# Kernel optimization log

Hardware: AMD Instinct MI355X
Metric: run time of the kernel (lower is better)

The kernel has to match this reference:

```python
import jax, jax.numpy as jnp
import numpy as np

NJ = 24
COL = 14
TMP = 3  # gaussian half-window (tmp_size)


def _forward(o, h, o3D, h3D, t, t3D, v):
    B = h.shape[0]
    f32 = jnp.float32
    scale = 1.0 / COL
    cc = COL * COL

    # ---- 2D heatmap argmax decode: x[i,j] = offset at argmax + coord*scale ----
    am = jnp.argmax(h.reshape(B, NJ, cc), axis=-1)            # (B, Nj)
    y2 = am // COL
    x2 = am % COL
    of = o.reshape(B, 2 * NJ, cc)
    gx = jnp.take_along_axis(of[:, :NJ], am[..., None], axis=-1)[..., 0]
    gy = jnp.take_along_axis(of[:, NJ:], am[..., None], axis=-1)[..., 0]
    x2d = jnp.stack([gx + x2.astype(f32) * scale,
                     gy + y2.astype(f32) * scale], axis=-1)   # (B, Nj, 2)

    # ---- 3D heatmap argmax decode ----
    h3r = h3D.reshape(B, NJ, COL, COL, COL)                   # (B, Nj, z, y, x)
    am3 = jnp.argmax(h3r.reshape(B, NJ, COL ** 3), axis=-1)
    z3 = am3 // cc
    r3 = am3 % cc
    y3 = r3 // COL
    x3 = r3 % COL
    o3r = o3D.reshape(B, 3, NJ, COL ** 3)                     # 3 coord channels
    g0 = jnp.take_along_axis(o3r[:, 0], am3[..., None], axis=-1)[..., 0]
    g1 = jnp.take_along_axis(o3r[:, 1], am3[..., None], axis=-1)[..., 0]
    g2 = jnp.take_along_axis(o3r[:, 2], am3[..., None], axis=-1)[..., 0]
    x3d = jnp.stack([g0 + x3.astype(f32) * scale,
                     g1 + y3.astype(f32) * scale,
                     g2 + (z3 - 7).astype(f32) * scale], axis=-1)  # (B, Nj, 3)

    v0 = v[..., 0]
    vis = (v0 == 1)

    # ---- 2D gaussian target placement (torch int() == floor for t >= 0) ----
    mu_x = jnp.floor(t[..., 0] * COL + 0.5).astype(jnp.int32)
    mu_y = jnp.floor(t[..., 1] * COL + 0.5).astype(jnp.int32)
    valid2d = ~((mu_x - TMP >= COL) | (mu_y - TMP >= COL) |
                (mu_x + TMP + 1 <= 0) | (mu_y + TMP + 1 <= 0))
    coords = jnp.arange(COL, dtype=jnp.int32)
    dx = coords[None, None, :] - mu_x[..., None]              # (B, Nj, COL)
    dy = coords[None, None, :] - mu_y[..., None]
    in2 = (jnp.abs(dx) <= TMP)[:, :, None, :] & (jnp.abs(dy) <= TMP)[:, :, :, None]
    sq2 = (dx.astype(f32) ** 2)[:, :, None, :] + (dy.astype(f32) ** 2)[:, :, :, None]
    gate2 = (vis & valid2d)[..., None, None]
    tt = jnp.where(in2 & gate2, jnp.exp(-0.5 * sq2), 0.0)     # (B, Nj, COL, COL)

    # ---- 3D gaussian target placement (only checked when still visible) ----
    m3x = jnp.floor(t3D[..., 0] * COL + 0.5).astype(jnp.int32)
    m3y = jnp.floor(t3D[..., 1] * COL + 0.5).astype(jnp.int32)
    m3z = jnp.floor(t3D[..., 2] * COL + 7 + 0.5).astype(jnp.int32)
    valid3d = ~((m3x - TMP >= COL) | (m3y - TMP >= COL) | (m3z - TMP >= COL) |
                (m3x + TMP + 1 < 0) | (m3y + TMP + 1 < 0) | (m3z + TMP + 1 < 0))
    dX = coords[None, None, :] - m3x[..., None]
    dY = coords[None, None, :] - m3y[..., None]
    dZ = coords[None, None, :] - m3z[..., None]
    in3 = ((jnp.abs(dX) <= TMP)[:, :, None, None, :] &
           (jnp.abs(dY) <= TMP)[:, :, None, :, None] &
           (jnp.abs(dZ) <= TMP)[:, :, :, None, None])
    sq3 = ((dX.astype(f32) ** 2)[:, :, None, None, :] +
           (dY.astype(f32) ** 2)[:, :, None, :, None] +
           (dZ.astype(f32) ** 2)[:, :, :, None, None])
    vf_bool = vis & valid2d & valid3d                          # final visibility
    tt3 = jnp.where(in3 & vf_bool[..., None, None, None], jnp.exp(-0.5 * sq3), 0.0)

    # ---- visibility mutation: v zeroed when a visible joint's target is OOB ----
    keep = jnp.where(vis, valid2d & valid3d, True)
    v_f = v * keep[..., None].astype(f32)                      # (B, Nj, 3)
    # x3D was skipped (left 0) when the 2D check invalidated a visible joint
    x3d = x3d * (~(vis & ~valid2d))[..., None].astype(f32)

    vf0 = v_f[..., 0]
    jmask = (vf0 != 0).astype(f32)                             # (B, Nj)
    cnt = jnp.sum(jmask)
    Nv = jnp.sum(v_f) / 3.0

    diff1 = (h - tt) * jmask[..., None, None]
    d1 = jnp.sqrt(jnp.sum(diff1 * diff1)) / cnt

    diff2 = (x2d - t) * v_f[..., :2]
    d2 = jnp.sqrt(jnp.sum(diff2 * diff2)) / Nv

    diff3 = (h3r - tt3) * jmask[..., None, None, None]
    d3 = jnp.sqrt(jnp.sum(diff3 * diff3)) / cnt

    diff4 = (x3d - t3D) * v_f
    d4 = jnp.sqrt(jnp.sum(diff4 * diff4)) / Nv

    return d1 + d2 + d3 + d4


def setup_inputs() -> dict:
    B = 256
    key = jax.random.key(0)
    ks = jax.random.split(key, 7)
    o = 0.1 * jax.random.normal(ks[0], (B, 2 * NJ, COL, COL), jnp.float32)
    h = jax.random.normal(ks[1], (B, NJ, COL, COL), jnp.float32)
    o3D = 0.1 * jax.random.normal(ks[2], (B, 3 * NJ * COL, COL, COL), jnp.float32)
    h3D = jax.random.normal(ks[3], (B, NJ * COL, COL, COL), jnp.float32)
    t = jax.random.uniform(ks[4], (B, NJ, 2), jnp.float32)
    t3D = jax.random.uniform(ks[5], (B, NJ, 3), jnp.float32)
    v0 = jax.random.bernoulli(ks[6], 0.8, (B, NJ)).astype(jnp.float32)
    v = jnp.repeat(v0[..., None], 3, axis=-1)
    return {"o": o, "h": h, "o3D": o3D, "h3D": h3D, "t": t, "t3D": t3D,
            "v": v, "d": 0, "path": 0}


def reference(o, h, o3D, h3D, t, t3D, v, d, path):
    # d > -990 selects the full d1+d2+d3+d4 loss (static Python branch)
    return _forward(o, h, o3D, h3D, t, t3D, v)
```

## Files before the change

### kernel.cpp

```cpp
#include <hip/hip_runtime.h>
#include <float.h>
#include <math.h>

#define NJ   24
#define COL  14
#define CC   196
#define CC3  2744
#define NV4_3D 686
#define NV4_2D 49
#define TMPW 3

__global__ __launch_bounds__(64)
void msed_pair_kernel(const float* __restrict__ o,
                      const float* __restrict__ h,
                      const float* __restrict__ o3D,
                      const float* __restrict__ h3D,
                      const float* __restrict__ t,
                      const float* __restrict__ t3D,
                      const float* __restrict__ v,
                      float* __restrict__ part)
{
    const int pair = blockIdx.x;
    const int lane = threadIdx.x;

    const float tx  = t[pair * 2 + 0];
    const float ty  = t[pair * 2 + 1];
    const float t3x = t3D[pair * 3 + 0];
    const float t3y = t3D[pair * 3 + 1];
    const float t3z = t3D[pair * 3 + 2];
    const float v0  = v[pair * 3 + 0];
    const float v1  = v[pair * 3 + 1];
    const float v2c = v[pair * 3 + 2];
    const bool vis = (v0 == 1.0f);

    const int mux = (int)floorf(tx * (float)COL + 0.5f);
    const int muy = (int)floorf(ty * (float)COL + 0.5f);
    const bool valid2d = !((mux - TMPW >= COL) || (muy - TMPW >= COL) ||
                           (mux + TMPW + 1 <= 0) || (muy + TMPW + 1 <= 0));

    const int m3x = (int)floorf(t3x * (float)COL + 0.5f);
    const int m3y = (int)floorf(t3y * (float)COL + 0.5f);
    const int m3z = (int)floorf(t3z * (float)COL + 7.0f + 0.5f);
    const bool valid3d = !((m3x - TMPW >= COL) || (m3y - TMPW >= COL) || (m3z - TMPW >= COL) ||
                           (m3x + TMPW + 1 < 0) || (m3y + TMPW + 1 < 0) || (m3z + TMPW + 1 < 0));

    const float keep = vis ? ((valid2d && valid3d) ? 1.0f : 0.0f) : 1.0f;
    const float vf0 = v0 * keep, vf1 = v1 * keep, vf2 = v2c * keep;
    const bool jm     = (vf0 != 0.0f);
    const bool active = jm || (vf1 != 0.0f) || (vf2 != 0.0f);
    const bool gate2  = vis && valid2d;
    const bool gate3  = vis && valid2d && valid3d;

    if (!active) {
        if (lane == 0) {
            float4 z4 = make_float4(0.f, 0.f, 0.f, 0.f);
            *(float4*)(part + (size_t)pair * 8)     = z4;
            *(float4*)(part + (size_t)pair * 8 + 4) = z4;
        }
        return;
    }

    const float4* hp3 = (const float4*)(h3D + (size_t)pair * CC3);
    float s3 = 0.0f;
    float bv3 = -FLT_MAX; int bi3 = 0x7FFFFFFF;
    #pragma unroll
    for (int u = 0; u < 11; ++u) {
        const int i = lane + (u << 6);
        const bool valid = (u < 10) || (lane < (NV4_3D - 640));
        const int ic = valid ? i : lane;
        float4 q = hp3[ic];
        float vals[4] = {q.x, q.y, q.z, q.w};
        const int e0 = ic * 4;
        #pragma unroll
        for (int c = 0; c < 4; ++c) {
            float hv = vals[c];
            if (valid) {
                s3 += hv * hv;
                if (hv > bv3) { bv3 = hv; bi3 = e0 + c; }
            }
        }
    }

    float s1 = 0.0f;
    float bv2 = -FLT_MAX; int bi2 = 0x7FFFFFFF;
    if (lane < NV4_2D) {
        const float4* hp2 = (const float4*)(h + (size_t)pair * CC);
        float4 q = hp2[lane];
        float vals[4] = {q.x, q.y, q.z, q.w};
        const int e0 = lane * 4;
        #pragma unroll
        for (int c = 0; c < 4; ++c) {
            float hv = vals[c];
            s1 += hv * hv;
            if (hv > bv2) { bv2 = hv; bi2 = e0 + c; }
        }
    }

    if (lane < 49) {
        const int dx = lane % 7 - TMPW;
        const int dy = lane / 7 - TMPW;
        const float gxy = __expf(-0.5f * (float)(dx * dx + dy * dy));

        if (gate2) {
            const int x = mux + dx, y = muy + dy;
            if ((unsigned)x < COL && (unsigned)y < COL) {
                const float wh = h[(size_t)pair * CC + y * COL + x];
                s1 += gxy * (gxy - 2.0f * wh);
            }
        }
        if (gate3) {
            const int x = m3x + dx, y = m3y + dy;
            if ((unsigned)x < COL && (unsigned)y < COL) {
                const float* base = h3D + (size_t)pair * CC3 + y * COL + x;
                #pragma unroll
                for (int dz = -TMPW; dz <= TMPW; ++dz) {
                    const int z = m3z + dz;
                    if ((unsigned)z < COL) {
                        const float g = gxy * __expf(-0.5f * (float)(dz * dz));
                        const float wh = base[z * CC];
                        s3 += g * (g - 2.0f * wh);
                    }
                }
            }
        }
    }

    #pragma unroll
    for (int off = 32; off > 0; off >>= 1) {
        s3 += __shfl_down(s3, off);
        s1 += __shfl_down(s1, off);
        float ov = __shfl_down(bv3, off); int oi = __shfl_down(bi3, off);
        if (ov > bv3 || (ov == bv3 && oi < bi3)) { bv3 = ov; bi3 = oi; }
        float ow = __shfl_down(bv2, off); int oj = __shfl_down(bi2, off);
        if (ow > bv2 || (ow == bv2 && oj < bi2)) { bv2 = ow; bi2 = oj; }
    }

    if (lane == 0) {
        const int b = pair / NJ;
        const int j = pair - b * NJ;
        const float scale = 1.0f / (float)COL;

        const int am = bi2;
        const int x2 = am % COL, y2 = am / COL;
        float gx = o[((size_t)b * (2 * NJ) + j) * CC + am];
        float gy = o[((size_t)b * (2 * NJ) + NJ + j) * CC + am];
        float x2dx = gx + (float)x2 * scale;
        float x2dy = gy + (float)y2 * scale;

        const int am3 = bi3;
        const int z3 = am3 / CC; const int r3 = am3 - z3 * CC;
        const int y3 = r3 / COL; const int x3 = r3 - y3 * COL;
        size_t base3 = (size_t)b * (3 * NJ * CC3) + (size_t)j * CC3 + am3;
        float g0 = o3D[base3];
        float g1 = o3D[base3 + (size_t)NJ * CC3];
        float g2 = o3D[base3 + (size_t)(2 * NJ) * CC3];
        float x3dx = g0 + (float)x3 * scale;
        float x3dy = g1 + (float)y3 * scale;
        float x3dz = g2 + (float)(z3 - 7) * scale;
        if (vis && !valid2d) { x3dx = 0.f; x3dy = 0.f; x3dz = 0.f; }

        float d2x = (x2dx - tx) * vf0;
        float d2y = (x2dy - ty) * vf1;
        float s2 = d2x * d2x + d2y * d2y;

        float d4x = (x3dx - t3x) * vf0;
        float d4y = (x3dy - t3y) * vf1;
        float d4z = (x3dz - t3z) * vf2;
        float s4 = d4x * d4x + d4y * d4y + d4z * d4z;

        float jmf = jm ? 1.0f : 0.0f;
        float4 p0 = make_float4(jm ? s1 : 0.f, s2, jm ? s3 : 0.f, s4);
        float4 p1 = make_float4(jmf, vf0 + vf1 + vf2, 0.f, 0.f);
        *(float4*)(part + (size_t)pair * 8)     = p0;
        *(float4*)(part + (size_t)pair * 8 + 4) = p1;
    }
}

__global__ __launch_bounds__(1024)
void msed_reduce_kernel(const float* __restrict__ part, int npairs,
                        float* __restrict__ out)
{
    const int tid = threadIdx.x;
    double a0 = 0, a1 = 0, a2 = 0, a3 = 0, a4 = 0, a5 = 0;
    for (int p = tid; p < npairs; p += 1024) {
        const float4 q0 = *(const float4*)(part + (size_t)p * 8);
        const float4 q1 = *(const float4*)(part + (size_t)p * 8 + 4);
        a0 += (double)q0.x; a1 += (double)q0.y; a2 += (double)q0.z; a3 += (double)q0.w;
        a4 += (double)q1.x; a5 += (double)q1.y;
    }

    #pragma unroll
    for (int off = 32; off > 0; off >>= 1) {
        a0 += __shfl_down(a0, off);
        a1 += __shfl_down(a1, off);
        a2 += __shfl_down(a2, off);
        a3 += __shfl_down(a3, off);
        a4 += __shfl_down(a4, off);
        a5 += __shfl_down(a5, off);
    }

    __shared__ double ws[16][6];
    const int wave = tid >> 6;
    if ((tid & 63) == 0) {
        ws[wave][0] = a0; ws[wave][1] = a1; ws[wave][2] = a2;
        ws[wave][3] = a3; ws[wave][4] = a4; ws[wave][5] = a5;
    }
    __syncthreads();

    if (tid == 0) {
        #pragma unroll
        for (int w = 1; w < 16; ++w) {
            a0 += ws[w][0]; a1 += ws[w][1]; a2 += ws[w][2];
            a3 += ws[w][3]; a4 += ws[w][4]; a5 += ws[w][5];
        }
        double cnt = a4;
        double Nv  = a5 / 3.0;
        float d1 = (float)(sqrt(a0) / cnt);
        float d2 = (float)(sqrt(a1) / Nv);
        float d3 = (float)(sqrt(a2) / cnt);
        float d4 = (float)(sqrt(a3) / Nv);
        out[0] = d1 + d2 + d3 + d4;
    }
}

extern "C" void kernel_launch(void* const* d_in, const int* in_sizes, int n_in,
                              void* d_out, int out_size, void* d_ws, size_t ws_size,
                              hipStream_t stream)
{
    const float* o   = (const float*)d_in[0];
    const float* h   = (const float*)d_in[1];
    const float* o3D = (const float*)d_in[2];
    const float* h3D = (const float*)d_in[3];
    const float* t   = (const float*)d_in[4];
    const float* t3D = (const float*)d_in[5];
    const float* v   = (const float*)d_in[6];

    const int B = in_sizes[1] / (NJ * CC);
    const int npairs = B * NJ;
    float* part = (float*)d_ws;

    msed_pair_kernel<<<npairs, 64, 0, stream>>>(o, h, o3D, h3D, t, t3D, v, part);
    msed_reduce_kernel<<<1, 1024, 0, stream>>>(part, npairs, (float*)d_out);
}
```

Before: 23.32 us.

## Fuse pair and reduce kernels with last-block atomic reduction, 4 pairs per block

Merges the per-pair kernel and the single-block reduce kernel into one launch. Each 256-thread block handles four pairs (one per wave), sums them in shared memory, and writes one partial per block. An atomic counter picks the last block to finish, and that block does the final double-precision reduction. This removes a kernel launch and shrinks the partial array, but adds a memset launch, threadfences and a serial tail for the last block.

Result: slower. 57.38 us (+146.1%).

```diff
diff --git a/kernel.cpp b/kernel.cpp
--- a/kernel.cpp
+++ b/kernel.cpp
@@ -9,180 +9,204 @@
 #define NV4_3D 686
 #define NV4_2D 49
 #define TMPW 3
-
-__global__ __launch_bounds__(64)
-void msed_pair_kernel(const float* __restrict__ o,
-                      const float* __restrict__ h,
-                      const float* __restrict__ o3D,
-                      const float* __restrict__ h3D,
-                      const float* __restrict__ t,
-                      const float* __restrict__ t3D,
-                      const float* __restrict__ v,
-                      float* __restrict__ part)
+#define PPB  4
+
+__global__ __launch_bounds__(256)
+void msed_fused_kernel(const float* __restrict__ o,
+                       const float* __restrict__ h,
+                       const float* __restrict__ o3D,
+                       const float* __restrict__ h3D,
+                       const float* __restrict__ t,
+                       const float* __restrict__ t3D,
+                       const float* __restrict__ v,
+                       float* __restrict__ part,
+                       unsigned int* __restrict__ counter,
+                       float* __restrict__ out,
+                       int npairs, int nblocks)
 {
-    const int pair = blockIdx.x;
-    const int lane = threadIdx.x;
-
-    const float tx  = t[pair * 2 + 0];
-    const float ty  = t[pair * 2 + 1];
-    const float t3x = t3D[pair * 3 + 0];
-    const float t3y = t3D[pair * 3 + 1];
-    const float t3z = t3D[pair * 3 + 2];
-    const float v0  = v[pair * 3 + 0];
-    const float v1  = v[pair * 3 + 1];
-    const float v2c = v[pair * 3 + 2];
-    const bool vis = (v0 == 1.0f);
-
-    const int mux = (int)floorf(tx * (float)COL + 0.5f);
-    const int muy = (int)floorf(ty * (float)COL + 0.5f);
-    const bool valid2d = !((mux - TMPW >= COL) || (muy - TMPW >= COL) ||
-                           (mux + TMPW + 1 <= 0) || (muy + TMPW + 1 <= 0));
-
-    const int m3x = (int)floorf(t3x * (float)COL + 0.5f);
-    const int m3y = (int)floorf(t3y * (float)COL + 0.5f);
-    const int m3z = (int)floorf(t3z * (float)COL + 7.0f + 0.5f);
-    const bool valid3d = !((m3x - TMPW >= COL) || (m3y - TMPW >= COL) || (m3z - TMPW >= COL) ||
-                           (m3x + TMPW + 1 < 0) || (m3y + TMPW + 1 < 0) || (m3z + TMPW + 1 < 0));
-
-    const float keep = vis ? ((valid2d && valid3d) ? 1.0f : 0.0f) : 1.0f;
-    const float vf0 = v0 * keep, vf1 = v1 * keep, vf2 = v2c * keep;
-    const bool jm     = (vf0 != 0.0f);
-    const bool active = jm || (vf1 != 0.0f) || (vf2 != 0.0f);
-    const bool gate2  = vis && valid2d;
-    const bool gate3  = vis && valid2d && valid3d;
-
-    if (!active) {
-        if (lane == 0) {
-            float4 z4 = make_float4(0.f, 0.f, 0.f, 0.f);
-            *(float4*)(part + (size_t)pair * 8)     = z4;
-            *(float4*)(part + (size_t)pair * 8 + 4) = z4;
+    const int wv   = threadIdx.x >> 6;
+    const int lane = threadIdx.x & 63;
+    const int pair = blockIdx.x * PPB + wv;
+
+    __shared__ float warr[PPB][6];
+    __shared__ int   lastFlag;
+
+    float p0 = 0.f, p1 = 0.f, p2 = 0.f, p3 = 0.f, p4 = 0.f, p5 = 0.f;
+
+    if (pair < npairs) {
+        const float tx  = t[pair * 2 + 0];
+        const float ty  = t[pair * 2 + 1];
+        const float t3x = t3D[pair * 3 + 0];
+        const float t3y = t3D[pair * 3 + 1];
+        const float t3z = t3D[pair * 3 + 2];
+        const float v0  = v[pair * 3 + 0];
+        const float v1  = v[pair * 3 + 1];
+        const float v2c = v[pair * 3 + 2];
+        const bool vis = (v0 == 1.0f);
+
+        const int mux = (int)floorf(tx * (float)COL + 0.5f);
+        const int muy = (int)floorf(ty * (float)COL + 0.5f);
+        const bool valid2d = !((mux - TMPW >= COL) || (muy - TMPW >= COL) ||
+                               (mux + TMPW + 1 <= 0) || (muy + TMPW + 1 <= 0));
+
+        const int m3x = (int)floorf(t3x * (float)COL + 0.5f);
+        const int m3y = (int)floorf(t3y * (float)COL + 0.5f);
+        const int m3z = (int)floorf(t3z * (float)COL + 7.0f + 0.5f);
+        const bool valid3d = !((m3x - TMPW >= COL) || (m3y - TMPW >= COL) || (m3z - TMPW >= COL) ||
+                               (m3x + TMPW + 1 < 0) || (m3y + TMPW + 1 < 0) || (m3z + TMPW + 1 < 0));
+
+        const float keep = vis ? ((valid2d && valid3d) ? 1.0f : 0.0f) : 1.0f;
+        const float vf0 = v0 * keep, vf1 = v1 * keep, vf2 = v2c * keep;
+        const bool jm     = (vf0 != 0.0f);
+        const bool active = jm || (vf1 != 0.0f) || (vf2 != 0.0f);
+        const bool gate2  = vis && valid2d;
+        const bool gate3  = vis && valid2d && valid3d;
+
+        if (active) {
+            const float4* hp3 = (const float4*)(h3D + (size_t)pair * CC3);
+            float s3 = 0.0f;
+            float bv3 = -FLT_MAX; int bi3 = 0x7FFFFFFF;
+            #pragma unroll
+            for (int u = 0; u < 11; ++u) {
+                const int i = lane + (u << 6);
+                const bool valid = (u < 10) || (lane < (NV4_3D - 640));
+                const int ic = valid ? i : lane;
+                float4 q = hp3[ic];
+                float vals[4] = {q.x, q.y, q.z, q.w};
+                const int e0 = ic * 4;
+                #pragma unroll
+                for (int c = 0; c < 4; ++c) {
+                    float hv = vals[c];
+                    if (valid) {
+                        s3 += hv * hv;
+                        if (hv > bv3) { bv3 = hv; bi3 = e0 + c; }
+                    }
+                }
+            }
+
+            float s1 = 0.0f;
+            float bv2 = -FLT_MAX; int bi2 = 0x7FFFFFFF;
+            if (lane < NV4_2D) {
+                const float4* hp2 = (const float4*)(h + (size_t)pair * CC);
+                float4 q = hp2[lane];
+                float vals[4] = {q.x, q.y, q.z, q.w};
+                const int e0 = lane * 4;
+                #pragma unroll
+                for (int c = 0; c < 4; ++c) {
+                    float hv = vals[c];
+                    s1 += hv * hv;
+                    if (hv > bv2) { bv2 = hv; bi2 = e0 + c; }
+                }
+            }
+
+            if (lane < 49) {
+                const int dx = lane % 7 - TMPW;
+                const int dy = lane / 7 - TMPW;
+                const float gxy = __expf(-0.5f * (float)(dx * dx + dy * dy));
+
+                if (gate2) {
+                    const int x = mux + dx, y = muy + dy;
+                    if ((unsigned)x < COL && (unsigned)y < COL) {
+                        const float wh = h[(size_t)pair * CC + y * COL + x];
+                        s1 += gxy * (gxy - 2.0f * wh);
+                    }
+                }
+                if (gate3) {
+                    const int x = m3x + dx, y = m3y + dy;
+                    if ((unsigned)x < COL && (unsigned)y < COL) {
+                        const float* base = h3D + (size_t)pair * CC3 + y * COL + x;
+                        #pragma unroll
+                        for (int dz = -TMPW; dz <= TMPW; ++dz) {
+                            const int z = m3z + dz;
+                            if ((unsigned)z < COL) {
+                                const float g = gxy * __expf(-0.5f * (float)(dz * dz));
+                                const float wh = base[z * CC];
+                                s3 += g * (g - 2.0f * wh);
+                            }
+                        }
+                    }
+                }
+            }
+
+            #pragma unroll
+            for (int off = 32; off > 0; off >>= 1) {
+                s3 += __shfl_down(s3, off);
+                s1 += __shfl_down(s1, off);
+                float ov = __shfl_down(bv3, off); int oi = __shfl_down(bi3, off);
+                if (ov > bv3 || (ov == bv3 && oi < bi3)) { bv3 = ov; bi3 = oi; }
+                float ow = __shfl_down(bv2, off); int oj = __shfl_down(bi2, off);
+                if (ow > bv2 || (ow == bv2 && oj < bi2)) { bv2 = ow; bi2 = oj; }
+            }
+
+            if (lane == 0) {
+                const int b = pair / NJ;
+                const int j = pair - b * NJ;
+                const float scale = 1.0f / (float)COL;
+
+                const int am = bi2;
+                const int x2 = am % COL, y2 = am / COL;
+                float gx = o[((size_t)b * (2 * NJ) + j) * CC + am];
+                float gy = o[((size_t)b * (2 * NJ) + NJ + j) * CC + am];
+                float x2dx = gx + (float)x2 * scale;
+                float x2dy = gy + (float)y2 * scale;
+
+                const int am3 = bi3;
+                const int z3 = am3 / CC; const int r3 = am3 - z3 * CC;
+                const int y3 = r3 / COL; const int x3 = r3 - y3 * COL;
+                size_t base3 = (size_t)b * (3 * NJ * CC3) + (size_t)j * CC3 + am3;
+                float g0 = o3D[base3];
+                float g1 = o3D[base3 + (size_t)NJ * CC3];
+                float g2 = o3D[base3 + (size_t)(2 * NJ) * CC3];
+                float x3dx = g0 + (float)x3 * scale;
+                float x3dy = g1 + (float)y3 * scale;
+                float x3dz = g2 + (float)(z3 - 7) * scale;
+                if (vis && !valid2d) { x3dx = 0.f; x3dy = 0.f; x3dz = 0.f; }
+
+                float d2x = (x2dx - tx) * vf0;
+                float d2y = (x2dy - ty) * vf1;
+                float s2 = d2x * d2x + d2y * d2y;
+
+                float d4x = (x3dx - t3x) * vf0;
+                float d4y = (x3dy - t3y) * vf1;
+                float d4z = (x3dz - t3z) * vf2;
+                float s4 = d4x * d4x + d4y * d4y + d4z * d4z;
+
+                p0 = jm ? s1 : 0.f;
+                p1 = s2;
+                p2 = jm ? s3 : 0.f;
+                p3 = s4;
+                p4 = jm ? 1.0f : 0.0f;
+                p5 = vf0 + vf1 + vf2;
+            }
         }
-        return;
-    }
-
-    const float4* hp3 = (const float4*)(h3D + (size_t)pair * CC3);
-    float s3 = 0.0f;
-    float bv3 = -FLT_MAX; int bi3 = 0x7FFFFFFF;
-    #pragma unroll
-    for (int u = 0; u < 11; ++u) {
-        const int i = lane + (u << 6);
-        const bool valid = (u < 10) || (lane < (NV4_3D - 640));
-        const int ic = valid ? i : lane;
-        float4 q = hp3[ic];
-        float vals[4] = {q.x, q.y, q.z, q.w};
-        const int e0 = ic * 4;
-        #pragma unroll
-        for (int c = 0; c < 4; ++c) {
-            float hv = vals[c];
-            if (valid) {
-                s3 += hv * hv;
-                if (hv > bv3) { bv3 = hv; bi3 = e0 + c; }
-            }
-        }
-    }
-
-    float s1 = 0.0f;
-    float bv2 = -FLT_MAX; int bi2 = 0x7FFFFFFF;
-    if (lane < NV4_2D) {
-        const float4* hp2 = (const float4*)(h + (size_t)pair * CC);
-        float4 q = hp2[lane];
-        float vals[4] = {q.x, q.y, q.z, q.w};
-        const int e0 = lane * 4;
-        #pragma unroll
-        for (int c = 0; c < 4; ++c) {
-            float hv = vals[c];
-            s1 += hv * hv;
-            if (hv > bv2) { bv2 = hv; bi2 = e0 + c; }
-        }
-    }
-
-    if (lane < 49) {
-        const int dx = lane % 7 - TMPW;
-        const int dy = lane / 7 - TMPW;
-        const float gxy = __expf(-0.5f * (float)(dx * dx + dy * dy));
-
-        if (gate2) {
-            const int x = mux + dx, y = muy + dy;
-            if ((unsigned)x < COL && (unsigned)y < COL) {
-                const float wh = h[(size_t)pair * CC + y * COL + x];
-                s1 += gxy * (gxy - 2.0f * wh);
-            }
-        }
-        if (gate3) {
-            const int x = m3x + dx, y = m3y + dy;
-            if ((unsigned)x < COL && (unsigned)y < COL) {
-                const float* base = h3D + (size_t)pair * CC3 + y * COL + x;
-                #pragma unroll
-                for (int dz = -TMPW; dz <= TMPW; ++dz) {
-                    const int z = m3z + dz;
-                    if ((unsigned)z < COL) {
-                        const float g = gxy * __expf(-0.5f * (float)(dz * dz));
-                        const float wh = base[z * CC];
-                        s3 += g * (g - 2.0f * wh);
-                    }
-                }
-            }
-        }
-    }
-
-    #pragma unroll
-    for (int off = 32; off > 0; off >>= 1) {
-        s3 += __shfl_down(s3, off);
-        s1 += __shfl_down(s1, off);
-        float ov = __shfl_down(bv3, off); int oi = __shfl_down(bi3, off);
-        if (ov > bv3 || (ov == bv3 && oi < bi3)) { bv3 = ov; bi3 = oi; }
-        float ow = __shfl_down(bv2, off); int oj = __shfl_down(bi2, off);
-        if (ow > bv2 || (ow == bv2 && oj < bi2)) { bv2 = ow; bi2 = oj; }
     }
 
     if (lane == 0) {
-        const int b = pair / NJ;
-        const int j = pair - b * NJ;
-        const float scale = 1.0f / (float)COL;
-
-        const int am = bi2;
-        const int x2 = am % COL, y2 = am / COL;
-        float gx = o[((size_t)b * (2 * NJ) + j) * CC + am];
-        float gy = o[((size_t)b * (2 * NJ) + NJ + j) * CC + am];
-        float x2dx = gx + (float)x2 * scale;
-        float x2dy = gy + (float)y2 * scale;
-
-        const int am3 = bi3;
-        const int z3 = am3 / CC; const int r3 = am3 - z3 * CC;
-        const int y3 = r3 / COL; const int x3 = r3 - y3 * COL;
-        size_t base3 = (size_t)b * (3 * NJ * CC3) + (size_t)j * CC3 + am3;
-        float g0 = o3D[base3];
-        float g1 = o3D[base3 + (size_t)NJ * CC3];
-        float g2 = o3D[base3 + (size_t)(2 * NJ) * CC3];
-        float x3dx = g0 + (float)x3 * scale;
-        float x3dy = g1 + (float)y3 * scale;
-        float x3dz = g2 + (float)(z3 - 7) * scale;
-        if (vis && !valid2d) { x3dx = 0.f; x3dy = 0.f; x3dz = 0.f; }
-
-        float d2x = (x2dx - tx) * vf0;
-        float d2y = (x2dy - ty) * vf1;
-        float s2 = d2x * d2x + d2y * d2y;
-
-        float d4x = (x3dx - t3x) * vf0;
-        float d4y = (x3dy - t3y) * vf1;
-        float d4z = (x3dz - t3z) * vf2;
-        float s4 = d4x * d4x + d4y * d4y + d4z * d4z;
-
-        float jmf = jm ? 1.0f : 0.0f;
-        float4 p0 = make_float4(jm ? s1 : 0.f, s2, jm ? s3 : 0.f, s4);
-        float4 p1 = make_float4(jmf, vf0 + vf1 + vf2, 0.f, 0.f);
-        *(float4*)(part + (size_t)pair * 8)     = p0;
-        *(float4*)(part + (size_t)pair * 8 + 4) = p1;
-    }
-}
-
-__global__ __launch_bounds__(1024)
-void msed_reduce_kernel(const float* __restrict__ part, int npairs,
-                        float* __restrict__ out)
-{
+        warr[wv][0] = p0; warr[wv][1] = p1; warr[wv][2] = p2;
+        warr[wv][3] = p3; warr[wv][4] = p4; warr[wv][5] = p5;
+    }
+    __syncthreads();
+
+    if (threadIdx.x == 0) {
+        float b0 = ((warr[0][0] + warr[1][0]) + warr[2][0]) + warr[3][0];
+        float b1 = ((warr[0][1] + warr[1][1]) + warr[2][1]) + warr[3][1];
+        float b2 = ((warr[0][2] + warr[1][2]) + warr[2][2]) + warr[3][2];
+        float b3 = ((warr[0][3] + warr[1][3]) + warr[2][3]) + warr[3][3];
+        float b4 = ((warr[0][4] + warr[1][4]) + warr[2][4]) + warr[3][4];
+        float b5 = ((warr[0][5] + warr[1][5]) + warr[2][5]) + warr[3][5];
+        *(float4*)(part + (size_t)blockIdx.x * 8)     = make_float4(b0, b1, b2, b3);
+        *(float4*)(part + (size_t)blockIdx.x * 8 + 4) = make_float4(b4, b5, 0.f, 0.f);
+        __threadfence();
+        unsigned old = atomicAdd(counter, 1u);
+        lastFlag = (old == (unsigned)(nblocks - 1)) ? 1 : 0;
+    }
+    __syncthreads();
+    if (!lastFlag) return;
+
+    __threadfence();
     const int tid = threadIdx.x;
     double a0 = 0, a1 = 0, a2 = 0, a3 = 0, a4 = 0, a5 = 0;
-    for (int p = tid; p < npairs; p += 1024) {
+    for (int p = tid; p < nblocks; p += 256) {
         const float4 q0 = *(const float4*)(part + (size_t)p * 8);
         const float4 q1 = *(const float4*)(part + (size_t)p * 8 + 4);
         a0 += (double)q0.x; a1 += (double)q0.y; a2 += (double)q0.z; a3 += (double)q0.w;
@@ -199,19 +223,19 @@
         a5 += __shfl_down(a5, off);
     }
 
-    __shared__ double ws[16][6];
+    __shared__ double ws2[4][6];
     const int wave = tid >> 6;
     if ((tid & 63) == 0) {
-        ws[wave][0] = a0; ws[wave][1] = a1; ws[wave][2] = a2;
-        ws[wave][3] = a3; ws[wave][4] = a4; ws[wave][5] = a5;
+        ws2[wave][0] = a0; ws2[wave][1] = a1; ws2[wave][2] = a2;
+        ws2[wave][3] = a3; ws2[wave][4] = a4; ws2[wave][5] = a5;
     }
     __syncthreads();
 
     if (tid == 0) {
         #pragma unroll
-        for (int w = 1; w < 16; ++w) {
-            a0 += ws[w][0]; a1 += ws[w][1]; a2 += ws[w][2];
-            a3 += ws[w][3]; a4 += ws[w][4]; a5 += ws[w][5];
+        for (int w = 1; w < 4; ++w) {
+            a0 += ws2[w][0]; a1 += ws2[w][1]; a2 += ws2[w][2];
+            a3 += ws2[w][3]; a4 += ws2[w][4]; a5 += ws2[w][5];
         }
         double cnt = a4;
         double Nv  = a5 / 3.0;
@@ -236,9 +260,14 @@
     const float* v   = (const float*)d_in[6];
 
     const int B = in_sizes[1] / (NJ * CC);
-    const int npairs = B * NJ;
+    const int npairs  = B * NJ;
+    const int nblocks = (npairs + PPB - 1) / PPB;
+
     float* part = (float*)d_ws;
-
-    msed_pair_kernel<<<npairs, 64, 0, stream>>>(o, h, o3D, h3D, t, t3D, v, part);
-    msed_reduce_kernel<<<1, 1024, 0, stream>>>(part, npairs, (float*)d_out);
+    unsigned int* counter = (unsigned int*)((char*)d_ws + (size_t)nblocks * 8 * sizeof(float));
+
+    hipMemsetAsync(counter, 0, sizeof(unsigned int), stream);
+    msed_fused_kernel<<<nblocks, 256, 0, stream>>>(o, h, o3D, h3D, t, t3D, v,
+                                                   part, counter, (float*)d_out,
+                                                   npairs, nblocks);
 }
```

## Use four waves per joint pair with shared-memory cross-wave argmax reduction

Applied to the files above, without the earlier changes.

Each (batch, joint) block grows from one wave to four, so every thread loads about three float4s of the 3D heatmap instead of eleven. The 7x7x7 gaussian window is spread as one cell per thread rather than a serial z loop per lane. A shared-memory stage combines the per-wave sums and argmax candidates before lane 0 writes its outputs. The aim is more memory-level parallelism per pair, at the cost of a __syncthreads and more threads sitting idle on the small 2D work.

Measured after the change: 25.94 us. +11.2%, slower.

```diff
diff --git a/kernel.cpp b/kernel.cpp
--- a/kernel.cpp
+++ b/kernel.cpp
@@ -1,6 +1,7 @@
 #include <hip/hip_runtime.h>
 #include <float.h>
 #include <math.h>
+#include <limits.h>
 
 #define NJ   24
 #define COL  14
@@ -10,7 +11,7 @@
 #define NV4_2D 49
 #define TMPW 3
 
-__global__ __launch_bounds__(64)
+__global__ __launch_bounds__(256)
 void msed_pair_kernel(const float* __restrict__ o,
                       const float* __restrict__ h,
                       const float* __restrict__ o3D,
@@ -21,7 +22,12 @@
                       float* __restrict__ part)
 {
     const int pair = blockIdx.x;
-    const int lane = threadIdx.x;
+    const int tid  = threadIdx.x;
+    const int lane = tid & 63;
+    const int wv   = tid >> 6;
+
+    __shared__ float wredf[4][4];
+    __shared__ int   wredi[4][2];
 
     const float tx  = t[pair * 2 + 0];
     const float ty  = t[pair * 2 + 1];
@@ -52,7 +58,7 @@
     const bool gate3  = vis && valid2d && valid3d;
 
     if (!active) {
-        if (lane == 0) {
+        if (tid == 0) {
             float4 z4 = make_float4(0.f, 0.f, 0.f, 0.f);
             *(float4*)(part + (size_t)pair * 8)     = z4;
             *(float4*)(part + (size_t)pair * 8 + 4) = z4;
@@ -60,66 +66,79 @@
         return;
     }
 
-    const float4* hp3 = (const float4*)(h3D + (size_t)pair * CC3);
-    float s3 = 0.0f;
-    float bv3 = -FLT_MAX; int bi3 = 0x7FFFFFFF;
-    #pragma unroll
-    for (int u = 0; u < 11; ++u) {
-        const int i = lane + (u << 6);
-        const bool valid = (u < 10) || (lane < (NV4_3D - 640));
-        const int ic = valid ? i : lane;
-        float4 q = hp3[ic];
+    float s3 = 0.0f, s1 = 0.0f;
+    float bv3 = -FLT_MAX, bv2 = -FLT_MAX;
+    int   bi3 = INT_MAX,  bi2 = INT_MAX;
+
+    {
+        const float4* hp3 = (const float4*)(h3D + (size_t)pair * CC3);
+        const bool has2 = (tid + 512) < NV4_3D;
+        float4 q0 = hp3[tid];
+        float4 q1 = hp3[tid + 256];
+        float4 q2 = hp3[has2 ? (tid + 512) : tid];
+
+        float a0[4] = {q0.x, q0.y, q0.z, q0.w};
+        float a1[4] = {q1.x, q1.y, q1.z, q1.w};
+        float a2[4] = {q2.x, q2.y, q2.z, q2.w};
+        #pragma unroll
+        for (int c = 0; c < 4; ++c) {
+            float hv = a0[c];
+            s3 += hv * hv;
+            if (hv > bv3) { bv3 = hv; bi3 = tid * 4 + c; }
+        }
+        #pragma unroll
+        for (int c = 0; c < 4; ++c) {
+            float hv = a1[c];
+            s3 += hv * hv;
+            if (hv > bv3) { bv3 = hv; bi3 = (tid + 256) * 4 + c; }
+        }
+        if (has2) {
+            #pragma unroll
+            for (int c = 0; c < 4; ++c) {
+                float hv = a2[c];
+                s3 += hv * hv;
+                if (hv > bv3) { bv3 = hv; bi3 = (tid + 512) * 4 + c; }
+            }
+        }
+    }
+
+    if (tid < NV4_2D) {
+        const float4* hp2 = (const float4*)(h + (size_t)pair * CC);
+        float4 q = hp2[tid];
         float vals[4] = {q.x, q.y, q.z, q.w};
-        const int e0 = ic * 4;
-        #pragma unroll
-        for (int c = 0; c < 4; ++c) {
-            float hv = vals[c];
-            if (valid) {
-                s3 += hv * hv;
-                if (hv > bv3) { bv3 = hv; bi3 = e0 + c; }
-            }
-        }
-    }
-
-    float s1 = 0.0f;
-    float bv2 = -FLT_MAX; int bi2 = 0x7FFFFFFF;
-    if (lane < NV4_2D) {
-        const float4* hp2 = (const float4*)(h + (size_t)pair * CC);
-        float4 q = hp2[lane];
-        float vals[4] = {q.x, q.y, q.z, q.w};
-        const int e0 = lane * 4;
         #pragma unroll
         for (int c = 0; c < 4; ++c) {
             float hv = vals[c];
             s1 += hv * hv;
-            if (hv > bv2) { bv2 = hv; bi2 = e0 + c; }
-        }
-    }
-
-    if (lane < 49) {
-        const int dx = lane % 7 - TMPW;
-        const int dy = lane / 7 - TMPW;
-        const float gxy = __expf(-0.5f * (float)(dx * dx + dy * dy));
-
-        if (gate2) {
-            const int x = mux + dx, y = muy + dy;
-            if ((unsigned)x < COL && (unsigned)y < COL) {
-                const float wh = h[(size_t)pair * CC + y * COL + x];
-                s1 += gxy * (gxy - 2.0f * wh);
-            }
-        }
-        if (gate3) {
-            const int x = m3x + dx, y = m3y + dy;
-            if ((unsigned)x < COL && (unsigned)y < COL) {
-                const float* base = h3D + (size_t)pair * CC3 + y * COL + x;
-                #pragma unroll
-                for (int dz = -TMPW; dz <= TMPW; ++dz) {
-                    const int z = m3z + dz;
-                    if ((unsigned)z < COL) {
-                        const float g = gxy * __expf(-0.5f * (float)(dz * dz));
-                        const float wh = base[z * CC];
-                        s3 += g * (g - 2.0f * wh);
-                    }
+            if (hv > bv2) { bv2 = hv; bi2 = tid * 4 + c; }
+        }
+    }
+
+    if (gate2 && tid < 49) {
+        const int dx = tid % 7 - TMPW;
+        const int dy = tid / 7 - TMPW;
+        const int x = mux + dx, y = muy + dy;
+        if ((unsigned)x < COL && (unsigned)y < COL) {
+            const float gxy = __expf(-0.5f * (float)(dx * dx + dy * dy));
+            const float wh = h[(size_t)pair * CC + y * COL + x];
+            s1 += gxy * (gxy - 2.0f * wh);
+        }
+    }
+
+    if (gate3) {
+        #pragma unroll
+        for (int r = 0; r < 2; ++r) {
+            const int cell = tid + r * 256;
+            if (cell < 343) {
+                const int dz = cell / 49 - TMPW;
+                const int rem = cell % 49;
+                const int dy = rem / 7 - TMPW;
+                const int dx = rem % 7 - TMPW;
+                const int x = m3x + dx, y = m3y + dy, z = m3z + dz;
+                if ((unsigned)x < COL && (unsigned)y < COL && (unsigned)z < COL) {
+                    const float g = __expf(-0.5f * (float)(dx * dx + dy * dy + dz * dz));
+                    const float wh = h3D[(size_t)pair * CC3 + z * CC + y * COL + x];
+                    s3 += g * (g - 2.0f * wh);
                 }
             }
         }
@@ -134,8 +153,24 @@
         float ow = __shfl_down(bv2, off); int oj = __shfl_down(bi2, off);
         if (ow > bv2 || (ow == bv2 && oj < bi2)) { bv2 = ow; bi2 = oj; }
     }
-
     if (lane == 0) {
+        wredf[wv][0] = s3; wredf[wv][1] = s1;
+        wredf[wv][2] = bv3; wredf[wv][3] = bv2;
+        wredi[wv][0] = bi3; wredi[wv][1] = bi2;
+    }
+    __syncthreads();
+
+    if (tid == 0) {
+        #pragma unroll
+        for (int w = 1; w < 4; ++w) {
+            s3 += wredf[w][0];
+            s1 += wredf[w][1];
+            float ov = wredf[w][2]; int oi = wredi[w][0];
+            if (ov > bv3 || (ov == bv3 && oi < bi3)) { bv3 = ov; bi3 = oi; }
+            float ow = wredf[w][3]; int oj = wredi[w][1];
+            if (ow > bv2 || (ow == bv2 && oj < bi2)) { bv2 = ow; bi2 = oj; }
+        }
+
         const int b = pair / NJ;
         const int j = pair - b * NJ;
         const float scale = 1.0f / (float)COL;
@@ -168,9 +203,8 @@
         float d4z = (x3dz - t3z) * vf2;
         float s4 = d4x * d4x + d4y * d4y + d4z * d4z;
 
-        float jmf = jm ? 1.0f : 0.0f;
         float4 p0 = make_float4(jm ? s1 : 0.f, s2, jm ? s3 : 0.f, s4);
-        float4 p1 = make_float4(jmf, vf0 + vf1 + vf2, 0.f, 0.f);
+        float4 p1 = make_float4(jm ? 1.0f : 0.0f, vf0 + vf1 + vf2, 0.f, 0.f);
         *(float4*)(part + (size_t)pair * 8)     = p0;
         *(float4*)(part + (size_t)pair * 8 + 4) = p1;
     }
@@ -237,8 +271,9 @@
 
     const int B = in_sizes[1] / (NJ * CC);
     const int npairs = B * NJ;
+
     float* part = (float*)d_ws;
 
-    msed_pair_kernel<<<npairs, 64, 0, stream>>>(o, h, o3D, h3D, t, t3D, v, part);
+    msed_pair_kernel<<<npairs, 256, 0, stream>>>(o, h, o3D, h3D, t, t3D, v, part);
     msed_reduce_kernel<<<1, 1024, 0, stream>>>(part, npairs, (float*)d_out);
 }
```
